# Kernel optimization log

Measured on AMD Instinct MI355X. Metric: run time of the kernel, lower is better.

Reference implementation:

```python
import jax, jax.numpy as jnp
import numpy as np

B = 2
C = 1024
H = 16
D = C // H  # 64
L_S, L_T, L_C = 2048, 1024, 512
MODS = ["shape", "texture", "color"]
SCALE_RMS = np.sqrt(D).astype(np.float32)
SCALE_ATTN = 1.0 / np.sqrt(D).astype(np.float32)


def _rms(x, gamma):
    # F.normalize(x, dim=-1) * gamma * sqrt(dim); x: [B,L,H,D], gamma: [H,D]
    n = jnp.linalg.norm(x, axis=-1, keepdims=True)
    return x / jnp.maximum(n, 1e-12) * gamma * SCALE_RMS


def _sdpa(q, k, v):
    # q: [B,Lq,H,D], k/v: [B,Lk,H,D] -> [B,Lq,H,D]
    s = jnp.einsum("blhd,bmhd->bhlm", q, k) * SCALE_ATTN
    a = jax.nn.softmax(s, axis=-1)
    return jnp.einsum("bhlm,bmhd->blhd", a, v)


def setup_inputs() -> dict:
    key = jax.random.key(0)
    ks = jax.random.split(key, 32)
    inp = {}
    lens = {"shape": L_S, "texture": L_T, "color": L_C}
    i = 0
    for m in MODS:
        inp[f"x_{m}"] = jax.random.normal(ks[i], (B, lens[m], C), jnp.float32); i += 1
        inp[f"Wqkv_{m}"] = jax.random.normal(ks[i], (C, 3 * C), jnp.float32) * 0.02; i += 1
        inp[f"bqkv_{m}"] = jnp.zeros((3 * C,), jnp.float32)
        inp[f"gq_{m}"] = jnp.ones((H, D), jnp.float32)
        inp[f"gk_{m}"] = jnp.ones((H, D), jnp.float32)
        inp[f"Wout_{m}"] = jax.random.normal(ks[i], (C, C), jnp.float32) * 0.02; i += 1
        inp[f"bout_{m}"] = jnp.zeros((C,), jnp.float32)
    return inp


def _forward(x_shape, x_texture, x_color,
             Wqkv_shape, bqkv_shape, gq_shape, gk_shape, Wout_shape, bout_shape,
             Wqkv_texture, bqkv_texture, gq_texture, gk_texture, Wout_texture, bout_texture,
             Wqkv_color, bqkv_color, gq_color, gk_color, Wout_color, bout_color):
    xs = {"shape": x_shape, "texture": x_texture, "color": x_color}
    Wqkv = {"shape": Wqkv_shape, "texture": Wqkv_texture, "color": Wqkv_color}
    bqkv = {"shape": bqkv_shape, "texture": bqkv_texture, "color": bqkv_color}
    gq = {"shape": gq_shape, "texture": gq_texture, "color": gq_color}
    gk = {"shape": gk_shape, "texture": gk_texture, "color": gk_color}
    Wout = {"shape": Wout_shape, "texture": Wout_texture, "color": Wout_color}
    bout = {"shape": bout_shape, "texture": bout_texture, "color": bout_color}

    q, k, v = {}, {}, {}
    for m in MODS:
        L = xs[m].shape[1]
        qkv = (xs[m] @ Wqkv[m] + bqkv[m]).reshape(B, L, 3, H, D)
        _q, _k, _v = qkv[:, :, 0], qkv[:, :, 1], qkv[:, :, 2]
        q[m] = _rms(_q, gq[m])
        k[m] = _rms(_k, gk[m])
        v[m] = _v

    # protected modality attends only to itself
    h = {"shape": _sdpa(q["shape"], k["shape"], v["shape"])}

    # other modalities: joint attention over [others ; detached protected]
    others = ["texture", "color"]
    q_o = jnp.concatenate([q[m] for m in others], axis=1)
    k_all = jnp.concatenate([k[m] for m in others] + [jax.lax.stop_gradient(k["shape"])], axis=1)
    v_all = jnp.concatenate([v[m] for m in others] + [jax.lax.stop_gradient(v["shape"])], axis=1)
    h_o = _sdpa(q_o, k_all, v_all)
    h["texture"] = h_o[:, :L_T]
    h["color"] = h_o[:, L_T:L_T + L_C]

    outs = []
    for m in MODS:
        L = h[m].shape[1]
        outs.append(h[m].reshape(B, L, C) @ Wout[m] + bout[m])
    return tuple(outs)


def reference(x_shape, x_texture, x_color,
              Wqkv_shape, bqkv_shape, gq_shape, gk_shape, Wout_shape, bout_shape,
              Wqkv_texture, bqkv_texture, gq_texture, gk_texture, Wout_texture, bout_texture,
              Wqkv_color, bqkv_color, gq_color, gk_color, Wout_color, bout_color):
    return _forward(x_shape, x_texture, x_color,
                    Wqkv_shape, bqkv_shape, gq_shape, gk_shape, Wout_shape, bout_shape,
                    Wqkv_texture, bqkv_texture, gq_texture, gk_texture, Wout_texture, bout_texture,
                    Wqkv_color, bqkv_color, gq_color, gk_color, Wout_color, bout_color)
```

## Files before the change

kernel.cpp:

```cpp
#include <hip/hip_runtime.h>
#include <hip/hip_bf16.h>
#include <stdint.h>

typedef unsigned short u16;
typedef unsigned int u32;
typedef __attribute__((ext_vector_type(8))) short bf16x8;
typedef __attribute__((ext_vector_type(4))) float f32x4;
typedef __attribute__((ext_vector_type(2))) unsigned int u32x2;
typedef __attribute__((ext_vector_type(4))) unsigned short u16x4;
typedef __attribute__((ext_vector_type(8))) unsigned short u16x8;

#define DEV __device__ __forceinline__

DEV u16 f2bf(float f){
  unsigned u = __float_as_uint(f);
  return (u16)((u + 0x7FFFu + ((u >> 16) & 1u)) >> 16);
}
DEV float b2f(u16 v){ return __uint_as_float(((unsigned)v) << 16); }

DEV u32 cvtpk(float lo, float hi){
  u32 r;
  asm("v_cvt_pk_bf16_f32 %0, %1, %2" : "=v"(r) : "v"(lo), "v"(hi));
  return r;
}

DEV f32x4 MFMA(bf16x8 a, bf16x8 b, f32x4 c){
  return __builtin_amdgcn_mfma_f32_16x16x32_bf16(a, b, c, 0, 0, 0);
}

__global__ __launch_bounds__(256) void cvt_f32_bf16(const float* __restrict__ in,
                                                    u16* __restrict__ out, int n4){
  int i = blockIdx.x * 256 + threadIdx.x;
  if (i >= n4) return;
  f32x4 v = ((const f32x4*)in)[i];
  u16x4 o;
  o[0] = f2bf(v[0]); o[1] = f2bf(v[1]); o[2] = f2bf(v[2]); o[3] = f2bf(v[3]);
  ((u16x4*)out)[i] = o;
}

__global__ __launch_bounds__(256) void tcvt(const float* __restrict__ in, u16* __restrict__ out,
                                            int R, int C){
  __shared__ float tile[64][65];
  int c0 = blockIdx.x * 64, r0 = blockIdx.y * 64;
  int t = threadIdx.x;
#pragma unroll
  for (int j = 0; j < 16; j++){
    int idx = j * 256 + t;
    int r = idx >> 6, c = idx & 63;
    tile[r][c] = in[(size_t)(r0 + r) * C + c0 + c];
  }
  __syncthreads();
#pragma unroll
  for (int j = 0; j < 16; j++){
    int idx = j * 256 + t;
    int c = idx >> 6, r = idx & 63;
    out[(size_t)(c0 + c) * R + r0 + r] = f2bf(tile[r][c]);
  }
}

template<int F32OUT>
__global__ __launch_bounds__(256) void gemm_bt(const u16* __restrict__ A, const u16* __restrict__ Bt,
                                               const float* __restrict__ bias, void* __restrict__ outp,
                                               int M, int N, int K){
  __shared__ __align__(16) u16 smA[128 * 40];
  __shared__ __align__(16) u16 smB[128 * 40];
  int t = threadIdx.x;
  int lane = t & 63, w = t >> 6;
  int wr = w >> 1, wc = w & 1;
  int li = lane & 15, g = lane >> 4;
  int m0 = blockIdx.y * 128, n0 = blockIdx.x * 128;

  int srow = t >> 2, sseg = (t & 3) * 8;
  const u16* Ap0 = A  + (size_t)(m0 + srow) * K + sseg;
  const u16* Ap1 = Ap0 + (size_t)64 * K;
  const u16* Bp0 = Bt + (size_t)(n0 + srow) * K + sseg;
  const u16* Bp1 = Bp0 + (size_t)64 * K;

  f32x4 acc[4][4] = {};
  u16x8 a0 = *(const u16x8*)Ap0, a1 = *(const u16x8*)Ap1;
  u16x8 b0 = *(const u16x8*)Bp0, b1 = *(const u16x8*)Bp1;

  for (int kt = 32; kt <= K; kt += 32){
    __syncthreads();
    *(u16x8*)&smA[srow * 40 + sseg]        = a0;
    *(u16x8*)&smA[(64 + srow) * 40 + sseg] = a1;
    *(u16x8*)&smB[srow * 40 + sseg]        = b0;
    *(u16x8*)&smB[(64 + srow) * 40 + sseg] = b1;
    __syncthreads();
    if (kt < K){
      a0 = *(const u16x8*)(Ap0 + kt); a1 = *(const u16x8*)(Ap1 + kt);
      b0 = *(const u16x8*)(Bp0 + kt); b1 = *(const u16x8*)(Bp1 + kt);
    }
    bf16x8 af[4], bfr[4];
#pragma unroll
    for (int mf = 0; mf < 4; mf++)
      af[mf] = *(const bf16x8*)&smA[(wr * 64 + mf * 16 + li) * 40 + g * 8];
#pragma unroll
    for (int nf = 0; nf < 4; nf++)
      bfr[nf] = *(const bf16x8*)&smB[(wc * 64 + nf * 16 + li) * 40 + g * 8];
#pragma unroll
    for (int mf = 0; mf < 4; mf++)
#pragma unroll
      for (int nf = 0; nf < 4; nf++)
        acc[mf][nf] = MFMA(af[mf], bfr[nf], acc[mf][nf]);
  }

#pragma unroll
  for (int mf = 0; mf < 4; mf++){
    int row = m0 + wr * 64 + mf * 16 + g * 4;
#pragma unroll
    for (int nf = 0; nf < 4; nf++){
      int col = n0 + wc * 64 + nf * 16 + li;
      float bs = bias[col];
#pragma unroll
      for (int r = 0; r < 4; r++){
        float v = acc[mf][nf][r] + bs;
        if (F32OUT) ((float*)outp)[(size_t)(row + r) * N + col] = v;
        else        ((u16*)outp)[(size_t)(row + r) * N + col]  = f2bf(v);
      }
    }
  }
}

__global__ __launch_bounds__(256) void rms_scatter(const u16* __restrict__ qkvb, int L,
                                                   const float* __restrict__ gq, const float* __restrict__ gk,
                                                   u16* __restrict__ qdst, int qL, int qoff,
                                                   u16* __restrict__ kdst, int kvoff){
  int tok = blockIdx.x;
  int b = tok / L, l = tok - b * L;
  int t = threadIdx.x;
  int c = t * 4;
  int h = t >> 4;
  int d = c & 63;
  const u16* rowq = qkvb + (size_t)tok * 3072 + c;
  u16x4 qv = *(const u16x4*)rowq;
  u16x4 kv = *(const u16x4*)(rowq + 1024);
  float qf[4], kf[4], ssq = 0.f, ssk = 0.f;
#pragma unroll
  for (int j = 0; j < 4; j++){
    qf[j] = b2f(qv[j]); kf[j] = b2f(kv[j]);
    ssq += qf[j] * qf[j]; ssk += kf[j] * kf[j];
  }
#pragma unroll
  for (int msk = 1; msk < 16; msk <<= 1){
    ssq += __shfl_xor(ssq, msk);
    ssk += __shfl_xor(ssk, msk);
  }
  float sq = 1.44269504088896340736f / fmaxf(sqrtf(ssq), 1e-12f);
  float sk = 8.0f / fmaxf(sqrtf(ssk), 1e-12f);
  u16x4 qo, ko;
#pragma unroll
  for (int j = 0; j < 4; j++){
    qo[j] = f2bf(qf[j] * sq * gq[h * 64 + d + j]);
    ko[j] = f2bf(kf[j] * sk * gk[h * 64 + d + j]);
  }
  *(u16x4*)(qdst + ((size_t)(b * 16 + h) * qL + qoff + l) * 64 + d) = qo;
  *(u16x4*)(kdst + ((size_t)(b * 16 + h) * 3584 + kvoff + l) * 64 + d) = ko;
}

__global__ __launch_bounds__(256) void vtrans(const u16* __restrict__ qkvb, int L,
                                              u16* __restrict__ vT, int kvoff){
  __shared__ u16 tile[64][65];
  int l0 = blockIdx.x * 64; int h = blockIdx.y; int b = blockIdx.z;
  int t = threadIdx.x;
#pragma unroll
  for (int j = 0; j < 16; j++){
    int idx = j * 256 + t;
    int r = idx >> 6, d = idx & 63;
    tile[r][d] = qkvb[(size_t)(b * L + l0 + r) * 3072 + 2048 + h * 64 + d];
  }
  __syncthreads();
#pragma unroll
  for (int j = 0; j < 16; j++){
    int idx = j * 256 + t;
    int d = idx >> 6, r = idx & 63;
    vT[((size_t)(b * 16 + h) * 64 + d) * 3584 + kvoff + l0 + r] = tile[r][d];
  }
}

__global__ __launch_bounds__(128, 3) void attn(const u16* __restrict__ q0, const u16* __restrict__ q1,
                                               const u16* __restrict__ kmat, const u16* __restrict__ vTm,
                                               u16* __restrict__ ob0, u16* __restrict__ ob1,
                                               u16* __restrict__ ob2){
  __shared__ __align__(16) u16 smK[64 * 72];
  __shared__ __align__(16) u16 smV[64 * 72];
  __shared__ __align__(16) u16 smP[2][32 * 68];
  int lin = blockIdx.x;
  bool t1 = lin < 768;
  int rel = t1 ? lin : lin - 768;
  int qb = rel >> 5, hb = rel & 31;
  int h = hb & 15, b = hb >> 4;
  int bh = b * 16 + h;
  const u16* qp = t1 ? q1 : q0;
  int Lq  = t1 ? 1536 : 2048;
  int kvo = t1 ? 0    : 1536;
  int Lk  = t1 ? 3584 : 2048;
  u16* out0 = t1 ? ob1 : ob0;  int L0 = t1 ? 1024 : 2048;
  u16* out1 = t1 ? ob2 : ob0;  int L1 = t1 ? 512  : 2048;

  int t = threadIdx.x, lane = t & 63, w = t >> 6;
  int li = lane & 15, g = lane >> 4;

  const u16* qbase = qp + ((size_t)bh * Lq + qb * 64 + w * 32) * 64;
  bf16x8 qa[2][2];
#pragma unroll
  for (int qg = 0; qg < 2; qg++)
#pragma unroll
    for (int kh = 0; kh < 2; kh++)
      qa[qg][kh] = *(const bf16x8*)(qbase + (size_t)(qg * 16 + li) * 64 + kh * 32 + g * 8);

  f32x4 acc[2][4] = {};
  float mrunL[2] = {-3.0e38f, -3.0e38f};
  float lsumL[2] = {0.f, 0.f};

  const u16* kbase = kmat + ((size_t)bh * 3584 + kvo) * 64;
  const u16* vbase = vTm + (size_t)bh * 64 * 3584 + kvo;
  u16* pp = &smP[w][0];

  u16x8 ka[4], va[4];
#pragma unroll
  for (int j = 0; j < 4; j++){
    int u = t + j * 128; int ur = u >> 3, us = (u & 7) * 8;
    ka[j] = *(const u16x8*)(kbase + (size_t)ur * 64 + us);
    va[j] = *(const u16x8*)(vbase + (size_t)ur * 3584 + us);
  }

  for (int kt = 0; kt < Lk; kt += 64){
    __syncthreads();
#pragma unroll
    for (int j = 0; j < 4; j++){
      int u = t + j * 128; int ur = u >> 3, us = (u & 7) * 8;
      *(u16x8*)&smK[ur * 72 + us] = ka[j];
      *(u16x8*)&smV[ur * 72 + us] = va[j];
    }
    __syncthreads();
    if (kt + 64 < Lk){
#pragma unroll
      for (int j = 0; j < 4; j++){
        int u = t + j * 128; int ur = u >> 3, us = (u & 7) * 8;
        ka[j] = *(const u16x8*)(kbase + (size_t)(kt + 64 + ur) * 64 + us);
        va[j] = *(const u16x8*)(vbase + (size_t)ur * 3584 + kt + 64 + us);
      }
    }

    f32x4 sT[2][4];
    __builtin_amdgcn_s_setprio(1);
#pragma unroll
    for (int kg = 0; kg < 4; kg++){
      bf16x8 kf0 = *(const bf16x8*)&smK[(kg * 16 + li) * 72 + g * 8];
      bf16x8 kf1 = *(const bf16x8*)&smK[(kg * 16 + li) * 72 + 32 + g * 8];
#pragma unroll
      for (int qg = 0; qg < 2; qg++){
        f32x4 z = {};
        z = MFMA(kf0, qa[qg][0], z);
        sT[qg][kg] = MFMA(kf1, qa[qg][1], z);
      }
    }
    __builtin_amdgcn_s_setprio(0);

    float rm[2];
#pragma unroll
    for (int qg = 0; qg < 2; qg++){
      float m01 = fmaxf(fmaxf(sT[qg][0][0], sT[qg][0][1]), fmaxf(sT[qg][0][2], sT[qg][0][3]));
      float m23 = fmaxf(fmaxf(sT[qg][1][0], sT[qg][1][1]), fmaxf(sT[qg][1][2], sT[qg][1][3]));
      float m45 = fmaxf(fmaxf(sT[qg][2][0], sT[qg][2][1]), fmaxf(sT[qg][2][2], sT[qg][2][3]));
      float m67 = fmaxf(fmaxf(sT[qg][3][0], sT[qg][3][1]), fmaxf(sT[qg][3][2], sT[qg][3][3]));
      float v = fmaxf(fmaxf(m01, m23), fmaxf(m45, m67));
      v = fmaxf(v, __shfl_xor(v, 16));
      v = fmaxf(v, __shfl_xor(v, 32));
      rm[qg] = v;
    }

    if (__any((rm[0] > mrunL[0]) | (rm[1] > mrunL[1]))){
#pragma unroll
      for (int qg = 0; qg < 2; qg++){
        float mo = mrunL[qg];
        float mn = fmaxf(mo, rm[qg]);
        float al = __builtin_exp2f(mo - mn);
        mrunL[qg] = mn;
        lsumL[qg] *= al;
#pragma unroll
        for (int dt = 0; dt < 4; dt++)
#pragma unroll
          for (int r = 0; r < 4; r++) acc[qg][dt][r] *= al;
      }
    }

#pragma unroll
    for (int qg = 0; qg < 2; qg++){
      float mn = mrunL[qg];
      float ps = 0.f;
#pragma unroll
      for (int kg = 0; kg < 4; kg++){
        float p0 = __builtin_exp2f(sT[qg][kg][0] - mn);
        float p1 = __builtin_exp2f(sT[qg][kg][1] - mn);
        float p2 = __builtin_exp2f(sT[qg][kg][2] - mn);
        float p3 = __builtin_exp2f(sT[qg][kg][3] - mn);
        ps += (p0 + p1) + (p2 + p3);
        u32x2 pk; pk[0] = cvtpk(p0, p1); pk[1] = cvtpk(p2, p3);
        *(u32x2*)&pp[(qg * 16 + li) * 68 + kg * 16 + g * 4] = pk;
      }
      lsumL[qg] += ps;
    }

    bf16x8 pf[2][2];
#pragma unroll
    for (int qg = 0; qg < 2; qg++){
      pf[qg][0] = *(const bf16x8*)&pp[(qg * 16 + li) * 68 + g * 8];
      pf[qg][1] = *(const bf16x8*)&pp[(qg * 16 + li) * 68 + 32 + g * 8];
    }
    __builtin_amdgcn_s_setprio(1);
#pragma unroll
    for (int dt = 0; dt < 4; dt++){
      bf16x8 vf0 = *(const bf16x8*)&smV[(dt * 16 + li) * 72 + g * 8];
      bf16x8 vf1 = *(const bf16x8*)&smV[(dt * 16 + li) * 72 + 32 + g * 8];
#pragma unroll
      for (int qg = 0; qg < 2; qg++){
        acc[qg][dt] = MFMA(vf0, pf[qg][0], acc[qg][dt]);
        acc[qg][dt] = MFMA(vf1, pf[qg][1], acc[qg][dt]);
      }
    }
    __builtin_amdgcn_s_setprio(0);
  }

#pragma unroll
  for (int qg = 0; qg < 2; qg++){
    float ls = lsumL[qg];
    ls += __shfl_xor(ls, 16);
    ls += __shfl_xor(ls, 32);
    float inv = 1.0f / ls;
    int qi = qb * 64 + w * 32 + qg * 16 + li;
    u16* dst; size_t basei;
    if (qi < L0){ dst = out0; basei = ((size_t)(b * L0 + qi)) * 1024 + h * 64; }
    else        { dst = out1; basei = ((size_t)(b * L1 + (qi - L0))) * 1024 + h * 64; }
#pragma unroll
    for (int dt = 0; dt < 4; dt++){
      u16x4 o;
#pragma unroll
      for (int r = 0; r < 4; r++) o[r] = f2bf(acc[qg][dt][r] * inv);
      *(u16x4*)&dst[basei + dt * 16 + g * 4] = o;
    }
  }
}

extern "C" void kernel_launch(void* const* d_in, const int* in_sizes, int n_in,
                              void* d_out, int out_size, void* d_ws, size_t ws_size,
                              hipStream_t stream){
  (void)in_sizes; (void)n_in; (void)out_size; (void)ws_size;
  const float* x[3]    = {(const float*)d_in[0],  (const float*)d_in[7],  (const float*)d_in[14]};
  const float* Wqkv[3] = {(const float*)d_in[1],  (const float*)d_in[8],  (const float*)d_in[15]};
  const float* bqkv[3] = {(const float*)d_in[2],  (const float*)d_in[9],  (const float*)d_in[16]};
  const float* gq[3]   = {(const float*)d_in[3],  (const float*)d_in[10], (const float*)d_in[17]};
  const float* gk[3]   = {(const float*)d_in[4],  (const float*)d_in[11], (const float*)d_in[18]};
  const float* Wout[3] = {(const float*)d_in[5],  (const float*)d_in[12], (const float*)d_in[19]};
  const float* bout[3] = {(const float*)d_in[6],  (const float*)d_in[13], (const float*)d_in[20]};
  float* outp = (float*)d_out;

  const int Ms[3] = {4096, 2048, 1024};
  const int Ls[3] = {2048, 1024, 512};
  const int kvoffs[3] = {1536, 0, 1024};

  u16* base = (u16*)d_ws;
  size_t off = 0;
  auto nxt = [&](size_t e){ u16* r = base + off; off += e; return r; };
  u16* xbf[3];  for (int m = 0; m < 3; m++) xbf[m]  = nxt((size_t)Ms[m] * 1024);
  u16* WqT[3];  for (int m = 0; m < 3; m++) WqT[m]  = nxt((size_t)3072 * 1024);
  u16* WoT[3];  for (int m = 0; m < 3; m++) WoT[m]  = nxt((size_t)1024 * 1024);
  u16* qkvb[3]; for (int m = 0; m < 3; m++) qkvb[m] = nxt((size_t)Ms[m] * 3072);
  u16* qA = nxt((size_t)2 * 16 * 2048 * 64);
  u16* qB = nxt((size_t)2 * 16 * 1536 * 64);
  u16* kB = nxt((size_t)2 * 16 * 3584 * 64);
  u16* vT = WqT[0];
  u16* hb[3]; for (int m = 0; m < 3; m++) hb[m] = xbf[m];

  for (int m = 0; m < 3; m++){
    int n4 = Ms[m] * 1024 / 4;
    cvt_f32_bf16<<<n4 / 256, 256, 0, stream>>>(x[m], xbf[m], n4);
    tcvt<<<dim3(3072 / 64, 1024 / 64), 256, 0, stream>>>(Wqkv[m], WqT[m], 1024, 3072);
    tcvt<<<dim3(1024 / 64, 1024 / 64), 256, 0, stream>>>(Wout[m], WoT[m], 1024, 1024);
  }
  for (int m = 0; m < 3; m++)
    gemm_bt<0><<<dim3(3072 / 128, Ms[m] / 128), 256, 0, stream>>>(
        xbf[m], WqT[m], bqkv[m], qkvb[m], Ms[m], 3072, 1024);
  rms_scatter<<<Ms[0], 256, 0, stream>>>(qkvb[0], Ls[0], gq[0], gk[0], qA, 2048, 0,    kB, 1536);
  rms_scatter<<<Ms[1], 256, 0, stream>>>(qkvb[1], Ls[1], gq[1], gk[1], qB, 1536, 0,    kB, 0);
  rms_scatter<<<Ms[2], 256, 0, stream>>>(qkvb[2], Ls[2], gq[2], gk[2], qB, 1536, 1024, kB, 1024);
  for (int m = 0; m < 3; m++)
    vtrans<<<dim3(Ls[m] / 64, 16, 2), 256, 0, stream>>>(qkvb[m], Ls[m], vT, kvoffs[m]);
  attn<<<1792, 128, 0, stream>>>(qA, qB, kB, vT, hb[0], hb[1], hb[2]);
  float* outs[3] = {outp, outp + (size_t)4096 * 1024, outp + (size_t)6144 * 1024};
  for (int m = 0; m < 3; m++)
    gemm_bt<1><<<dim3(1024 / 128, Ms[m] / 128), 256, 0, stream>>>(
        hb[m], WoT[m], bout[m], outs[m], Ms[m], 1024, 1024);
}
```

Baseline: 542.4 us.

## Batch per-modality GEMMs into one launch and load tiles via global_load_lds

```diff
diff --git a/kernel.cpp b/kernel.cpp
--- a/kernel.cpp
+++ b/kernel.cpp
@@ -26,6 +26,11 @@
 
 DEV f32x4 MFMA(bf16x8 a, bf16x8 b, f32x4 c){
   return __builtin_amdgcn_mfma_f32_16x16x32_bf16(a, b, c, 0, 0, 0);
+}
+
+DEV void gload16(const u16* g, u16* l){
+  __builtin_amdgcn_global_load_lds((const __attribute__((address_space(1))) u32*)g,
+                                   (__attribute__((address_space(3))) u32*)l, 16, 0, 0);
 }
 
 __global__ __launch_bounds__(256) void cvt_f32_bf16(const float* __restrict__ in,
@@ -59,45 +64,58 @@
 }
 
 template<int F32OUT>
-__global__ __launch_bounds__(256) void gemm_bt(const u16* __restrict__ A, const u16* __restrict__ Bt,
-                                               const float* __restrict__ bias, void* __restrict__ outp,
-                                               int M, int N, int K){
-  __shared__ __align__(16) u16 smA[128 * 40];
-  __shared__ __align__(16) u16 smB[128 * 40];
+__global__ __launch_bounds__(256) void gemm3(const u16* __restrict__ A0, const u16* __restrict__ A1,
+                                             const u16* __restrict__ A2,
+                                             const u16* __restrict__ B0, const u16* __restrict__ B1,
+                                             const u16* __restrict__ B2,
+                                             const float* __restrict__ bi0, const float* __restrict__ bi1,
+                                             const float* __restrict__ bi2,
+                                             void* __restrict__ o0, void* __restrict__ o1,
+                                             void* __restrict__ o2,
+                                             int N, int K, int rb0, int rb1){
+  __shared__ __align__(16) u16 smA[128 * 32];
+  __shared__ __align__(16) u16 smB[128 * 32];
+  int yb = blockIdx.y;
+  const u16 *A, *Bt; const float* bias; void* outp;
+  int m0;
+  if (yb < rb0)            { A = A0; Bt = B0; bias = bi0; outp = o0; m0 = yb * 128; }
+  else if (yb < rb0 + rb1) { A = A1; Bt = B1; bias = bi1; outp = o1; m0 = (yb - rb0) * 128; }
+  else                     { A = A2; Bt = B2; bias = bi2; outp = o2; m0 = (yb - rb0 - rb1) * 128; }
+
   int t = threadIdx.x;
   int lane = t & 63, w = t >> 6;
   int wr = w >> 1, wc = w & 1;
   int li = lane & 15, g = lane >> 4;
-  int m0 = blockIdx.y * 128, n0 = blockIdx.x * 128;
-
-  int srow = t >> 2, sseg = (t & 3) * 8;
-  const u16* Ap0 = A  + (size_t)(m0 + srow) * K + sseg;
-  const u16* Ap1 = Ap0 + (size_t)64 * K;
-  const u16* Bp0 = Bt + (size_t)(n0 + srow) * K + sseg;
-  const u16* Bp1 = Bp0 + (size_t)64 * K;
+  int n0 = blockIdx.x * 128;
+
+  int srow = w * 32 + (lane >> 2);
+  int sk = (lane & 3) * 8;
+  const u16* Ag0 = A  + (size_t)(m0 + srow) * K + sk;
+  const u16* Ag1 = A  + (size_t)(m0 + srow + 16) * K + sk;
+  const u16* Bg0 = Bt + (size_t)(n0 + srow) * K + sk;
+  const u16* Bg1 = Bt + (size_t)(n0 + srow + 16) * K + sk;
+  u16* la0 = &smA[w * 1024];
+  u16* la1 = &smA[w * 1024 + 512];
+  u16* lb0 = &smB[w * 1024];
+  u16* lb1 = &smB[w * 1024 + 512];
 
   f32x4 acc[4][4] = {};
-  u16x8 a0 = *(const u16x8*)Ap0, a1 = *(const u16x8*)Ap1;
-  u16x8 b0 = *(const u16x8*)Bp0, b1 = *(const u16x8*)Bp1;
-
-  for (int kt = 32; kt <= K; kt += 32){
+
+  for (int kt = 0; kt < K; kt += 32){
     __syncthreads();
-    *(u16x8*)&smA[srow * 40 + sseg]        = a0;
-    *(u16x8*)&smA[(64 + srow) * 40 + sseg] = a1;
-    *(u16x8*)&smB[srow * 40 + sseg]        = b0;
-    *(u16x8*)&smB[(64 + srow) * 40 + sseg] = b1;
+    gload16(Ag0 + kt, la0);
+    gload16(Ag1 + kt, la1);
+    gload16(Bg0 + kt, lb0);
+    gload16(Bg1 + kt, lb1);
     __syncthreads();
-    if (kt < K){
-      a0 = *(const u16x8*)(Ap0 + kt); a1 = *(const u16x8*)(Ap1 + kt);
-      b0 = *(const u16x8*)(Bp0 + kt); b1 = *(const u16x8*)(Bp1 + kt);
-    }
+
     bf16x8 af[4], bfr[4];
 #pragma unroll
     for (int mf = 0; mf < 4; mf++)
-      af[mf] = *(const bf16x8*)&smA[(wr * 64 + mf * 16 + li) * 40 + g * 8];
+      af[mf] = *(const bf16x8*)&smA[(wr * 64 + mf * 16 + li) * 32 + g * 8];
 #pragma unroll
     for (int nf = 0; nf < 4; nf++)
-      bfr[nf] = *(const bf16x8*)&smB[(wc * 64 + nf * 16 + li) * 40 + g * 8];
+      bfr[nf] = *(const bf16x8*)&smB[(wc * 64 + nf * 16 + li) * 32 + g * 8];
 #pragma unroll
     for (int mf = 0; mf < 4; mf++)
 #pragma unroll
@@ -379,9 +397,10 @@
     tcvt<<<dim3(3072 / 64, 1024 / 64), 256, 0, stream>>>(Wqkv[m], WqT[m], 1024, 3072);
     tcvt<<<dim3(1024 / 64, 1024 / 64), 256, 0, stream>>>(Wout[m], WoT[m], 1024, 1024);
   }
-  for (int m = 0; m < 3; m++)
-    gemm_bt<0><<<dim3(3072 / 128, Ms[m] / 128), 256, 0, stream>>>(
-        xbf[m], WqT[m], bqkv[m], qkvb[m], Ms[m], 3072, 1024);
+  gemm3<0><<<dim3(3072 / 128, 56), 256, 0, stream>>>(
+      xbf[0], xbf[1], xbf[2], WqT[0], WqT[1], WqT[2],
+      bqkv[0], bqkv[1], bqkv[2], qkvb[0], qkvb[1], qkvb[2],
+      3072, 1024, 32, 16);
   rms_scatter<<<Ms[0], 256, 0, stream>>>(qkvb[0], Ls[0], gq[0], gk[0], qA, 2048, 0,    kB, 1536);
   rms_scatter<<<Ms[1], 256, 0, stream>>>(qkvb[1], Ls[1], gq[1], gk[1], qB, 1536, 0,    kB, 0);
   rms_scatter<<<Ms[2], 256, 0, stream>>>(qkvb[2], Ls[2], gq[2], gk[2], qB, 1536, 1024, kB, 1024);
@@ -389,7 +408,8 @@
     vtrans<<<dim3(Ls[m] / 64, 16, 2), 256, 0, stream>>>(qkvb[m], Ls[m], vT, kvoffs[m]);
   attn<<<1792, 128, 0, stream>>>(qA, qB, kB, vT, hb[0], hb[1], hb[2]);
   float* outs[3] = {outp, outp + (size_t)4096 * 1024, outp + (size_t)6144 * 1024};
-  for (int m = 0; m < 3; m++)
-    gemm_bt<1><<<dim3(1024 / 128, Ms[m] / 128), 256, 0, stream>>>(
-        hb[m], WoT[m], bout[m], outs[m], Ms[m], 1024, 1024);
-}
+  gemm3<1><<<dim3(1024 / 128, 56), 256, 0, stream>>>(
+      hb[0], hb[1], hb[2], WoT[0], WoT[1], WoT[2],
+      bout[0], bout[1], bout[2], outs[0], outs[1], outs[2],
+      1024, 1024, 32, 16);
+}
```

Result: faster. 500.3 us (-7.8%).
